# Optimization experiments

Hardware: AMD Instinct MI355X
Metric: run time of the kernel (lower is better)

## Reference

```python
import jax, jax.numpy as jnp
import numpy as np

DIM = 1024
DIM_QK = 1024
DIM_V = 1024
H = 16
SCALE = 1.0 / (DIM_QK ** 0.5)  # NOTE: module scales by sqrt(dim_qk), not sqrt(head_dim)


def setup_inputs() -> dict:
    key = jax.random.key(0)
    ks = jax.random.split(key, 12)
    B, S = 2, 2048
    q = jax.random.normal(ks[0], (B, S, DIM), jnp.float32)
    k = jax.random.normal(ks[1], (B, S, DIM), jnp.float32)
    v = jax.random.normal(ks[2], (B, S, DIM), jnp.float32)
    mask = jax.random.randint(ks[3], (B, 1, S, S), 0, 2) > 0  # True = masked
    s = 1.0 / np.sqrt(DIM)
    Wq = jax.random.uniform(ks[4], (DIM_QK, DIM), jnp.float32, -s, s)
    bq = jax.random.uniform(ks[5], (DIM_QK,), jnp.float32, -s, s)
    Wk = jax.random.uniform(ks[6], (DIM_QK, DIM), jnp.float32, -s, s)
    bk = jax.random.uniform(ks[7], (DIM_QK,), jnp.float32, -s, s)
    Wv = jax.random.uniform(ks[8], (DIM_V, DIM), jnp.float32, -s, s)
    bv = jax.random.uniform(ks[9], (DIM_V,), jnp.float32, -s, s)
    Wo = jax.random.uniform(ks[10], (DIM_V, DIM), jnp.float32, -s, s)
    bo = jax.random.uniform(ks[11], (DIM_V,), jnp.float32, -s, s)
    return {"q": q, "k": k, "v": v, "mask": mask,
            "Wq": Wq, "bq": bq, "Wk": Wk, "bk": bk,
            "Wv": Wv, "bv": bv, "Wo": Wo, "bo": bo}


def reference(q, k, v, mask, Wq, bq, Wk, bk, Wv, bv, Wo, bo):
    B, Sq, _ = q.shape
    Skv = k.shape[1]
    # projections (torch Linear: x @ W.T + b)
    qh = (q @ Wq.T + bq).reshape(B, Sq, H, DIM_QK // H).transpose(0, 2, 1, 3)   # [B,H,Sq,dk]
    kh = (k @ Wk.T + bk).reshape(B, Skv, H, DIM_QK // H).transpose(0, 2, 1, 3)  # [B,H,Skv,dk]
    vh = (v @ Wv.T + bv).reshape(B, Skv, H, DIM_V // H).transpose(0, 2, 1, 3)   # [B,H,Skv,dv]
    attn = jnp.einsum('bhqd,bhkd->bhqk', qh, kh) * SCALE
    attn = jnp.where(mask, jnp.float32(-1e20), attn)
    attn = jax.nn.softmax(attn, axis=-1)
    # dropout is identity in eval / p=0
    out = jnp.einsum('bhqk,bhkd->bhqd', attn, vh)            # [B,H,Sq,dv]
    out = out.transpose(0, 2, 1, 3).reshape(B, Sq, DIM_V)
    return out @ Wo.T + bo
```

## Files before the change

### kernel.cpp

```cpp
#include <hip/hip_runtime.h>
#include <hip/hip_bf16.h>

typedef __attribute__((ext_vector_type(8))) __bf16 bf16x8;
typedef __attribute__((ext_vector_type(4))) short short4v;
typedef __attribute__((ext_vector_type(4))) float f32x4;
typedef __attribute__((ext_vector_type(4))) unsigned int uint4v;
typedef __attribute__((ext_vector_type(2))) unsigned int uint2v;

#define S_LEN 2048
#define DIM_  1024
#define HDIM  64
#define SCALE2 0.045084441f

#define EXP2F(x) __builtin_amdgcn_exp2f(x)

#define ATTN_SWZ(row, col8) (((row) * 64) + (((col8) ^ ((row) & 7)) << 3))

__device__ __forceinline__ void async_copy16(const void* gp, void* lp) {
  __builtin_amdgcn_global_load_lds(
      (const __attribute__((address_space(1))) unsigned int*)gp,
      (__attribute__((address_space(3))) unsigned int*)lp, 16, 0, 0);
}

__device__ __forceinline__ unsigned f2bf_u(float f) {
  unsigned u = __builtin_bit_cast(unsigned, f);
  return (u + 0x7FFFu + ((u >> 16) & 1u)) >> 16;
}
__device__ __forceinline__ unsigned pack2(float a, float b) {
  return f2bf_u(a) | (f2bf_u(b) << 16);
}
__device__ __forceinline__ unsigned cvtpk(float a, float b) {
  float2 f; f.x = a; f.y = b;
  __hip_bfloat162 h = __float22bfloat162_rn(f);
  unsigned u;
  __builtin_memcpy(&u, &h, 4);
  return u;
}

__global__ __launch_bounds__(256) void cvt_kernel(
    const float* __restrict__ s0, const float* __restrict__ s1, const float* __restrict__ s2,
    const float* __restrict__ s3, const float* __restrict__ s4, const float* __restrict__ s5,
    const float* __restrict__ s6,
    __hip_bfloat16* __restrict__ d0, __hip_bfloat16* __restrict__ d1, __hip_bfloat16* __restrict__ d2,
    __hip_bfloat16* __restrict__ d3, __hip_bfloat16* __restrict__ d4, __hip_bfloat16* __restrict__ d5,
    __hip_bfloat16* __restrict__ d6,
    const int* __restrict__ mask, unsigned long long* __restrict__ bits)
{
  if (blockIdx.y == 7) {
    int wave = threadIdx.x >> 6, lane = threadIdx.x & 63;
    int gw = blockIdx.x * 4 + wave;
#pragma unroll
    for (int it = 0; it < 16; ++it) {
      int w = gw * 16 + it;
      int m = mask[(size_t)w * 64 + lane];
      unsigned long long bal = __ballot(m != 0);
      if (lane == 0) bits[w] = bal;
    }
    return;
  }
  const float* srcs[7] = {s0, s1, s2, s3, s4, s5, s6};
  __hip_bfloat16* dsts[7] = {d0, d1, d2, d3, d4, d5, d6};
  const int sizes[7] = {4194304, 4194304, 4194304, 1048576, 1048576, 1048576, 1048576};
  int rg = blockIdx.y;
  int base = (blockIdx.x * 256 + threadIdx.x) * 8;
  if (base >= sizes[rg]) return;
  const float* s = srcs[rg] + base;
  f32x4 a = *(const f32x4*)s;
  f32x4 b = *(const f32x4*)(s + 4);
  uint4v o;
  o.x = pack2(a[0], a[1]); o.y = pack2(a[2], a[3]);
  o.z = pack2(b[0], b[1]); o.w = pack2(b[2], b[3]);
  *(uint4v*)(dsts[rg] + base) = o;
}

__device__ __forceinline__ void swz(int r, int& m0, int& n0) {
  int c  = ((r & 7) << 2) | (r >> 6);
  int xl = (r >> 3) & 7;
  m0 = ((c >> 3) * 8 + xl) * 128;
  n0 = (c & 7) * 128;
}

__global__ __launch_bounds__(256) void qkv_gemm_kernel(
    const __hip_bfloat16* __restrict__ xq, const __hip_bfloat16* __restrict__ xk,
    const __hip_bfloat16* __restrict__ xv,
    const __hip_bfloat16* __restrict__ Wq, const float* __restrict__ bq,
    const __hip_bfloat16* __restrict__ Wk, const float* __restrict__ bk,
    const __hip_bfloat16* __restrict__ Wv, const float* __restrict__ bv,
    __hip_bfloat16* __restrict__ Q, __hip_bfloat16* __restrict__ Kk,
    __hip_bfloat16* __restrict__ VT)
{
  const __hip_bfloat16 *X, *W; const float* bias;
  if (blockIdx.z == 0)      { X = xq; W = Wq; bias = bq; }
  else if (blockIdx.z == 1) { X = xk; W = Wk; bias = bk; }
  else                      { X = xv; W = Wv; bias = bv; }

  constexpr int K = 1024, N = 1024;
  __shared__ alignas(16) __hip_bfloat16 As[2][128 * 32];
  __shared__ alignas(16) __hip_bfloat16 Bs[2][128 * 32];
  const int tid  = threadIdx.x;
  const int lane = tid & 63;
  const int wave = tid >> 6;
  const int t    = lane & 15;
  const int quad = lane >> 4;
  const int wm   = wave >> 1;
  const int wn   = wave & 1;
  int m0, n0;
  swz(blockIdx.x, m0, n0);

  f32x4 acc[4][4] = {};

  const int c0 = tid, c1 = 256 + tid;
  const int r0 = c0 >> 2, o0 = (c0 & 3) * 8;
  const int r1 = c1 >> 2, o1 = (c1 & 3) * 8;
  const __hip_bfloat16* xp0 = &X[(size_t)(m0 + r0) * K + o0];
  const __hip_bfloat16* xp1 = &X[(size_t)(m0 + r1) * K + o1];
  const __hip_bfloat16* wp0 = &W[(size_t)(n0 + r0) * K + o0];
  const __hip_bfloat16* wp1 = &W[(size_t)(n0 + r1) * K + o1];

  async_copy16(xp0, &As[0][c0 * 8]);
  async_copy16(xp1, &As[0][c1 * 8]);
  async_copy16(wp0, &Bs[0][c0 * 8]);
  async_copy16(wp1, &Bs[0][c1 * 8]);

  int buf = 0;
  for (int k0 = 0; k0 < K; k0 += 32) {
    __syncthreads();
    if (k0 + 32 < K) {
      int nb = buf ^ 1;
      int kn = k0 + 32;
      async_copy16(xp0 + kn, &As[nb][c0 * 8]);
      async_copy16(xp1 + kn, &As[nb][c1 * 8]);
      async_copy16(wp0 + kn, &Bs[nb][c0 * 8]);
      async_copy16(wp1 + kn, &Bs[nb][c1 * 8]);
    }
    bf16x8 a[4], b[4];
#pragma unroll
    for (int i = 0; i < 4; ++i)
      a[i] = *(const bf16x8*)&As[buf][(wm * 64 + i * 16 + t) * 32 + quad * 8];
#pragma unroll
    for (int j = 0; j < 4; ++j)
      b[j] = *(const bf16x8*)&Bs[buf][(wn * 64 + j * 16 + t) * 32 + quad * 8];
#pragma unroll
    for (int i = 0; i < 4; ++i)
#pragma unroll
      for (int j = 0; j < 4; ++j)
        acc[i][j] = __builtin_amdgcn_mfma_f32_16x16x32_bf16(a[i], b[j], acc[i][j], 0, 0, 0);
    buf ^= 1;
  }

  float bj[4];
#pragma unroll
  for (int j = 0; j < 4; ++j)
    bj[j] = bias[n0 + wn * 64 + j * 16 + t];

  if (blockIdx.z == 2) {
#pragma unroll
    for (int i = 0; i < 4; ++i)
#pragma unroll
      for (int j = 0; j < 4; ++j) {
        int m = m0 + wm * 64 + i * 16 + quad * 4;
        int n = n0 + wn * 64 + j * 16 + t;
        int bb = m >> 11, kv = m & 2047;
        int hh = n >> 6,  dv = n & 63;
        uint2v o;
        o.x = pack2(acc[i][j][0] + bj[j], acc[i][j][1] + bj[j]);
        o.y = pack2(acc[i][j][2] + bj[j], acc[i][j][3] + bj[j]);
        *(uint2v*)&VT[(size_t)(((bb * 16 + hh) * 64) + dv) * 2048 + kv] = o;
      }
  } else {
    const bool isq = (blockIdx.z == 0);
    __hip_bfloat16* Out = isq ? Q : Kk;
    const float sc = isq ? SCALE2 : 1.0f;
#pragma unroll
    for (int i = 0; i < 4; ++i)
#pragma unroll
      for (int j = 0; j < 4; ++j)
#pragma unroll
        for (int r = 0; r < 4; ++r) {
          int m = m0 + wm * 64 + i * 16 + quad * 4 + r;
          int n = n0 + wn * 64 + j * 16 + t;
          Out[(size_t)m * N + n] = __float2bfloat16((acc[i][j][r] + bj[j]) * sc);
        }
  }
}

__global__ __launch_bounds__(256) void proj_gemm_kernel(
    const __hip_bfloat16* __restrict__ X, const __hip_bfloat16* __restrict__ W,
    const float* __restrict__ bias, float* __restrict__ Out)
{
  constexpr int K = 1024, N = 1024;
  __shared__ alignas(16) __hip_bfloat16 As[2][128 * 32];
  __shared__ alignas(16) __hip_bfloat16 Bs[2][128 * 32];
  const int tid  = threadIdx.x;
  const int lane = tid & 63;
  const int wave = tid >> 6;
  const int t    = lane & 15;
  const int quad = lane >> 4;
  const int wm   = wave >> 1;
  const int wn   = wave & 1;
  int m0, n0;
  swz(blockIdx.x, m0, n0);

  f32x4 acc[4][4] = {};

  const int c0 = tid, c1 = 256 + tid;
  const int r0 = c0 >> 2, o0 = (c0 & 3) * 8;
  const int r1 = c1 >> 2, o1 = (c1 & 3) * 8;
  const __hip_bfloat16* xp0 = &X[(size_t)(m0 + r0) * K + o0];
  const __hip_bfloat16* xp1 = &X[(size_t)(m0 + r1) * K + o1];
  const __hip_bfloat16* wp0 = &W[(size_t)(n0 + r0) * K + o0];
  const __hip_bfloat16* wp1 = &W[(size_t)(n0 + r1) * K + o1];

  async_copy16(xp0, &As[0][c0 * 8]);
  async_copy16(xp1, &As[0][c1 * 8]);
  async_copy16(wp0, &Bs[0][c0 * 8]);
  async_copy16(wp1, &Bs[0][c1 * 8]);

  int buf = 0;
  for (int k0 = 0; k0 < K; k0 += 32) {
    __syncthreads();
    if (k0 + 32 < K) {
      int nb = buf ^ 1;
      int kn = k0 + 32;
      async_copy16(xp0 + kn, &As[nb][c0 * 8]);
      async_copy16(xp1 + kn, &As[nb][c1 * 8]);
      async_copy16(wp0 + kn, &Bs[nb][c0 * 8]);
      async_copy16(wp1 + kn, &Bs[nb][c1 * 8]);
    }
    bf16x8 a[4], b[4];
#pragma unroll
    for (int i = 0; i < 4; ++i)
      a[i] = *(const bf16x8*)&As[buf][(wm * 64 + i * 16 + t) * 32 + quad * 8];
#pragma unroll
    for (int j = 0; j < 4; ++j)
      b[j] = *(const bf16x8*)&Bs[buf][(wn * 64 + j * 16 + t) * 32 + quad * 8];
#pragma unroll
    for (int i = 0; i < 4; ++i)
#pragma unroll
      for (int j = 0; j < 4; ++j)
        acc[i][j] = __builtin_amdgcn_mfma_f32_16x16x32_bf16(a[i], b[j], acc[i][j], 0, 0, 0);
    buf ^= 1;
  }

  float bj[4];
#pragma unroll
  for (int j = 0; j < 4; ++j)
    bj[j] = bias[n0 + wn * 64 + j * 16 + t];
#pragma unroll
  for (int i = 0; i < 4; ++i)
#pragma unroll
    for (int j = 0; j < 4; ++j)
#pragma unroll
      for (int r = 0; r < 4; ++r) {
        int m = m0 + wm * 64 + i * 16 + quad * 4 + r;
        int n = n0 + wn * 64 + j * 16 + t;
        Out[(size_t)m * N + n] = acc[i][j][r] + bj[j];
      }
}

__global__ __launch_bounds__(256) void attn_kernel(
    const __hip_bfloat16* __restrict__ Qb,
    const __hip_bfloat16* __restrict__ Kb,
    const __hip_bfloat16* __restrict__ VT,
    const unsigned long long* __restrict__ mbits,
    __hip_bfloat16* __restrict__ Ob)
{
  const int bid = blockIdx.x;
  const int qt = (bid >> 3) & 31;
  const int g  = ((bid & 7) << 2) | (bid >> 8);
  const int h  = g & 15;
  const int b  = g >> 4;
  const int qb = qt * 64;

  __shared__ alignas(16) __hip_bfloat16 Qs[64 * 64];
  __shared__ alignas(16) __hip_bfloat16 Ks[2][64 * 64];
  __shared__ alignas(16) __hip_bfloat16 Vt[2][64 * 64];

  const int tid  = threadIdx.x;
  const int lane = tid & 63;
  const int wave = tid >> 6;
  const int t    = lane & 15;
  const int quad = lane >> 4;

  const int r0 = tid >> 3;
  const int r1 = 32 + r0;
  const int k0c = ((tid & 7) ^ (r0 & 7)) << 3;
  const int k1c = ((tid & 7) ^ (r1 & 7)) << 3;
  const __hip_bfloat16* kp0 = &Kb[((size_t)(b * S_LEN + r0)) * DIM_ + h * HDIM + k0c];
  const __hip_bfloat16* kp1 = &Kb[((size_t)(b * S_LEN + r1)) * DIM_ + h * HDIM + k1c];
  const size_t vtbase = (size_t)((b * 16 + h) * 64) * 2048;
  const __hip_bfloat16* vp0 = &VT[vtbase + (size_t)r0 * 2048 + k0c];
  const __hip_bfloat16* vp1 = &VT[vtbase + (size_t)r1 * 2048 + k1c];

  async_copy16(kp0, &Ks[0][tid * 8]);
  async_copy16(kp1, &Ks[0][(256 + tid) * 8]);
  async_copy16(vp0, &Vt[0][tid * 8]);
  async_copy16(vp1, &Vt[0][(256 + tid) * 8]);

#pragma unroll
  for (int r = 0; r < 2; ++r) {
    int c = r * 256 + tid;
    int row = c >> 3, c8 = c & 7;
    uint4 raw = *(const uint4*)&Qb[((size_t)(b * S_LEN + qb + row)) * DIM_ + h * HDIM + c8 * 8];
    *(uint4*)&Qs[ATTN_SWZ(row, c8)] = raw;
  }
  __syncthreads();

  bf16x8 qf[2];
#pragma unroll
  for (int ks = 0; ks < 2; ++ks)
    qf[ks] = *(const bf16x8*)&Qs[ATTN_SWZ(wave * 16 + t, ks * 4 + quad)];

  int koff[8];
#pragma unroll
  for (int i = 0; i < 4; ++i) {
    koff[i]     = ATTN_SWZ(i * 16 + t, quad);
    koff[4 + i] = ATTN_SWZ(i * 16 + t, 4 + quad);
  }
  int voff[16];
#pragma unroll
  for (int j = 0; j < 4; ++j)
#pragma unroll
    for (int n = 0; n < 4; ++n)
      voff[j * 4 + n] = (n * 16 + t) * 64 +
          (((j * 2 + (quad >> 1)) ^ (t & 7)) << 3) + (quad & 1) * 4;

  f32x4 lp4 = {0.f, 0.f, 0.f, 0.f};
  f32x4 o[4] = {};

  const int qg = qb + wave * 16 + t;
  const size_t mbase = ((size_t)b * S_LEN + qg) * 32;
  const int qshift = quad * 4;

#define ATTN_TILE(kvt, BUF)                                                   \
  {                                                                           \
    unsigned long long mw = mbits[mbase + (kvt)];                             \
    if ((kvt) > 0) __syncthreads();                \
    if ((kvt) + 1 < 32) {                                                     \
      size_t koffg = (size_t)((kvt) + 1) * 64 * DIM_;                         \
      int    voffg = ((kvt) + 1) * 64;                                        \
      async_copy16(kp0 + koffg, &Ks[(BUF) ^ 1][tid * 8]);                     \
      async_copy16(kp1 + koffg, &Ks[(BUF) ^ 1][(256 + tid) * 8]);             \
      async_copy16(vp0 + voffg, &Vt[(BUF) ^ 1][tid * 8]);                     \
      async_copy16(vp1 + voffg, &Vt[(BUF) ^ 1][(256 + tid) * 8]);             \
    }                                                                         \
    __builtin_amdgcn_s_setprio(1);                                            \
    unsigned long long mwq = mw >> qshift;                                    \
    unsigned mlo = (unsigned)mwq, mhi = (unsigned)(mwq >> 32);                \
    unsigned mqv[4] = {mlo & 0xFu, (mlo >> 16) & 0xFu,                        \
                       mhi & 0xFu, (mhi >> 16) & 0xFu};                       \
    float e[4][4];                                                            \
    _Pragma("unroll")                                                         \
    for (int i = 0; i < 4; ++i) {                                             \
      f32x4 z = {};                                                           \
      bf16x8 a0 = *(const bf16x8*)&Ks[BUF][koff[i]];                          \
      z = __builtin_amdgcn_mfma_f32_16x16x32_bf16(a0, qf[0], z, 0, 0, 0);     \
      bf16x8 a1 = *(const bf16x8*)&Ks[BUF][koff[4 + i]];                      \
      z = __builtin_amdgcn_mfma_f32_16x16x32_bf16(a1, qf[1], z, 0, 0, 0);     \
      _Pragma("unroll")                                                       \
      for (int r = 0; r < 4; ++r) {                                           \
        float v = ((mqv[i] >> r) & 1u) ? -1e20f : z[r];                       \
        float ex = EXP2F(v);                                                  \
        e[i][r] = ex;                                                         \
        lp4[r] += ex;                                                         \
      }                                                                       \
    }                                                                         \
    short4v pf[4];                                                            \
    _Pragma("unroll")                                                         \
    for (int j = 0; j < 4; ++j) {                                             \
      uint2v pk;                                                              \
      pk.x = cvtpk(e[j][0], e[j][1]);                                         \
      pk.y = cvtpk(e[j][2], e[j][3]);                                         \
      pf[j] = __builtin_bit_cast(short4v, pk);                                \
    }                                                                         \
    _Pragma("unroll")                                                         \
    for (int j = 0; j < 4; ++j)                                               \
      _Pragma("unroll")                                                       \
      for (int n = 0; n < 4; ++n) {                                           \
        short4v va = *(const short4v*)&Vt[BUF][voff[j * 4 + n]];              \
        o[n] = __builtin_amdgcn_mfma_f32_16x16x16bf16_1k(va, pf[j], o[n],     \
                                                         0, 0, 0);            \
      }                                                                       \
    __builtin_amdgcn_s_setprio(0);                                            \
  }

  ATTN_TILE(0, 0)
  for (int kvt = 1; kvt < 31; kvt += 2) {
    ATTN_TILE(kvt, 1)
    ATTN_TILE(kvt + 1, 0)
  }
  ATTN_TILE(31, 1)
#undef ATTN_TILE

  float lp = (lp4[0] + lp4[1]) + (lp4[2] + lp4[3]);
  lp += __shfl_xor(lp, 16, 64);
  lp += __shfl_xor(lp, 32, 64);
  float rl = 1.0f / lp;

  __hip_bfloat16* Ts = Qs;
  __syncthreads();
#pragma unroll
  for (int n = 0; n < 4; ++n) {
    uint2v pk;
    pk.x = cvtpk(o[n][0] * rl, o[n][1] * rl);
    pk.y = cvtpk(o[n][2] * rl, o[n][3] * rl);
    *(uint2v*)&Ts[(wave * 16 + t) * 64 +
                  (((n * 2 + (quad >> 1)) ^ (t & 7)) << 3) + (quad & 1) * 4] = pk;
  }
  __syncthreads();
  {
    int row = tid >> 2;
    int b0  = (tid & 3) * 2;
    uint4 x0 = *(const uint4*)&Ts[row * 64 + ((b0 ^ (row & 7)) << 3)];
    uint4 x1 = *(const uint4*)&Ts[row * 64 + (((b0 + 1) ^ (row & 7)) << 3)];
    int d0 = (tid & 3) * 16;
    __hip_bfloat16* dst = &Ob[((size_t)(b * S_LEN + qb + row)) * DIM_ + h * HDIM + d0];
    *(uint4*)dst = x0;
    *(uint4*)(dst + 8) = x1;
  }
}

extern "C" void kernel_launch(void* const* d_in, const int* in_sizes, int n_in,
                              void* d_out, int out_size, void* d_ws, size_t ws_size,
                              hipStream_t stream) {
  const float* q  = (const float*)d_in[0];
  const float* k  = (const float*)d_in[1];
  const float* v  = (const float*)d_in[2];
  const int*   mk = (const int*)d_in[3];
  const float* Wq = (const float*)d_in[4];
  const float* bq = (const float*)d_in[5];
  const float* Wk = (const float*)d_in[6];
  const float* bk = (const float*)d_in[7];
  const float* Wv = (const float*)d_in[8];
  const float* bv = (const float*)d_in[9];
  const float* Wo = (const float*)d_in[10];
  const float* bo = (const float*)d_in[11];
  float* out = (float*)d_out;

  char* ws = (char*)d_ws;
  const size_t MB = 1024 * 1024;
  __hip_bfloat16* Qb  = (__hip_bfloat16*)(ws);
  __hip_bfloat16* Kb  = (__hip_bfloat16*)(ws + 8  * MB);
  __hip_bfloat16* VTb = (__hip_bfloat16*)(ws + 16 * MB);
  __hip_bfloat16* Ob  = (__hip_bfloat16*)(ws + 24 * MB);
  __hip_bfloat16* xqb = (__hip_bfloat16*)(ws + 32 * MB);
  __hip_bfloat16* xkb = (__hip_bfloat16*)(ws + 40 * MB);
  __hip_bfloat16* xvb = (__hip_bfloat16*)(ws + 48 * MB);
  __hip_bfloat16* Wqb = (__hip_bfloat16*)(ws + 56 * MB);
  __hip_bfloat16* Wkb = (__hip_bfloat16*)(ws + 58 * MB);
  __hip_bfloat16* Wvb = (__hip_bfloat16*)(ws + 60 * MB);
  __hip_bfloat16* Wob = (__hip_bfloat16*)(ws + 62 * MB);
  unsigned long long* mbits = (unsigned long long*)(ws + 64 * MB);

  cvt_kernel<<<dim3(2048, 8), 256, 0, stream>>>(q, k, v, Wq, Wk, Wv, Wo,
                                                xqb, xkb, xvb, Wqb, Wkb, Wvb, Wob,
                                                mk, mbits);
  qkv_gemm_kernel<<<dim3(256, 1, 3), 256, 0, stream>>>(xqb, xkb, xvb,
                                                       Wqb, bq, Wkb, bk, Wvb, bv,
                                                       Qb, Kb, VTb);
  attn_kernel<<<dim3(1024), 256, 0, stream>>>(Qb, Kb, VTb, mbits, Ob);
  proj_gemm_kernel<<<dim3(256), 256, 0, stream>>>(Ob, Wob, bo, out);
}
```

Measured before the change: 260.6 us.

## Process 128 query rows per attention block to reuse K/V tiles

Each attention workgroup now covers 128 query rows instead of 64, with every wave handling two 16-row query sub-tiles that share the same K fragments and V loads from LDS. This halves the global K/V traffic and the LDS fragment reads per query row, and it halves the grid to 512 blocks. In exchange, register pressure rises from doubled accumulators and cached K fragments, and the smaller grid may underfill the 256 CUs.

```diff
diff --git a/kernel.cpp b/kernel.cpp
--- a/kernel.cpp
+++ b/kernel.cpp
@@ -266,13 +266,13 @@
     __hip_bfloat16* __restrict__ Ob)
 {
   const int bid = blockIdx.x;
-  const int qt = (bid >> 3) & 31;
-  const int g  = ((bid & 7) << 2) | (bid >> 8);
+  const int qt = (bid >> 3) & 15;
+  const int g  = ((bid & 7) << 2) | (bid >> 7);
   const int h  = g & 15;
   const int b  = g >> 4;
-  const int qb = qt * 64;
-
-  __shared__ alignas(16) __hip_bfloat16 Qs[64 * 64];
+  const int qb = qt * 128;
+
+  __shared__ alignas(16) __hip_bfloat16 Qs[128 * 64];
   __shared__ alignas(16) __hip_bfloat16 Ks[2][64 * 64];
   __shared__ alignas(16) __hip_bfloat16 Vt[2][64 * 64];
 
@@ -298,7 +298,7 @@
   async_copy16(vp1, &Vt[0][(256 + tid) * 8]);
 
 #pragma unroll
-  for (int r = 0; r < 2; ++r) {
+  for (int r = 0; r < 4; ++r) {
     int c = r * 256 + tid;
     int row = c >> 3, c8 = c & 7;
     uint4 raw = *(const uint4*)&Qb[((size_t)(b * S_LEN + qb + row)) * DIM_ + h * HDIM + c8 * 8];
@@ -306,10 +306,12 @@
   }
   __syncthreads();
 
-  bf16x8 qf[2];
-#pragma unroll
-  for (int ks = 0; ks < 2; ++ks)
-    qf[ks] = *(const bf16x8*)&Qs[ATTN_SWZ(wave * 16 + t, ks * 4 + quad)];
+  bf16x8 qf[2][2];
+#pragma unroll
+  for (int hh = 0; hh < 2; ++hh)
+#pragma unroll
+    for (int ks = 0; ks < 2; ++ks)
+      qf[hh][ks] = *(const bf16x8*)&Qs[ATTN_SWZ(wave * 32 + hh * 16 + t, ks * 4 + quad)];
 
   int koff[8];
 #pragma unroll
@@ -325,16 +327,19 @@
       voff[j * 4 + n] = (n * 16 + t) * 64 +
           (((j * 2 + (quad >> 1)) ^ (t & 7)) << 3) + (quad & 1) * 4;
 
-  f32x4 lp4 = {0.f, 0.f, 0.f, 0.f};
-  f32x4 o[4] = {};
-
-  const int qg = qb + wave * 16 + t;
-  const size_t mbase = ((size_t)b * S_LEN + qg) * 32;
+  f32x4 lpa = {0.f, 0.f, 0.f, 0.f};
+  f32x4 lpb = {0.f, 0.f, 0.f, 0.f};
+  f32x4 oa[4] = {};
+  f32x4 ob[4] = {};
+
+  const size_t mbase0 = ((size_t)b * S_LEN + qb + wave * 32 + t) * 32;
+  const size_t mbase1 = mbase0 + 16 * 32;
   const int qshift = quad * 4;
 
 #define ATTN_TILE(kvt, BUF)                                                   \
   {                                                                           \
-    unsigned long long mw = mbits[mbase + (kvt)];                             \
+    unsigned long long mw0 = mbits[mbase0 + (kvt)];                           \
+    unsigned long long mw1 = mbits[mbase1 + (kvt)];                           \
     if ((kvt) > 0) __syncthreads();                \
     if ((kvt) + 1 < 32) {                                                     \
       size_t koffg = (size_t)((kvt) + 1) * 64 * DIM_;                         \
@@ -345,41 +350,62 @@
       async_copy16(vp1 + voffg, &Vt[(BUF) ^ 1][(256 + tid) * 8]);             \
     }                                                                         \
     __builtin_amdgcn_s_setprio(1);                                            \
-    unsigned long long mwq = mw >> qshift;                                    \
-    unsigned mlo = (unsigned)mwq, mhi = (unsigned)(mwq >> 32);                \
-    unsigned mqv[4] = {mlo & 0xFu, (mlo >> 16) & 0xFu,                        \
-                       mhi & 0xFu, (mhi >> 16) & 0xFu};                       \
-    float e[4][4];                                                            \
+    unsigned long long mwq0 = mw0 >> qshift;                                  \
+    unsigned long long mwq1 = mw1 >> qshift;                                  \
+    unsigned m0lo = (unsigned)mwq0, m0hi = (unsigned)(mwq0 >> 32);            \
+    unsigned m1lo = (unsigned)mwq1, m1hi = (unsigned)(mwq1 >> 32);            \
+    unsigned mqv0[4] = {m0lo & 0xFu, (m0lo >> 16) & 0xFu,                     \
+                        m0hi & 0xFu, (m0hi >> 16) & 0xFu};                    \
+    unsigned mqv1[4] = {m1lo & 0xFu, (m1lo >> 16) & 0xFu,                     \
+                        m1hi & 0xFu, (m1hi >> 16) & 0xFu};                    \
+    bf16x8 kf[8];                                                             \
+    _Pragma("unroll")                                                         \
+    for (int i = 0; i < 4; ++i) {                                             \
+      kf[i]     = *(const bf16x8*)&Ks[BUF][koff[i]];                          \
+      kf[4 + i] = *(const bf16x8*)&Ks[BUF][koff[4 + i]];                      \
+    }                                                                         \
+    short4v pf0[4], pf1[4];                                                   \
     _Pragma("unroll")                                                         \
     for (int i = 0; i < 4; ++i) {                                             \
       f32x4 z = {};                                                           \
-      bf16x8 a0 = *(const bf16x8*)&Ks[BUF][koff[i]];                          \
-      z = __builtin_amdgcn_mfma_f32_16x16x32_bf16(a0, qf[0], z, 0, 0, 0);     \
-      bf16x8 a1 = *(const bf16x8*)&Ks[BUF][koff[4 + i]];                      \
-      z = __builtin_amdgcn_mfma_f32_16x16x32_bf16(a1, qf[1], z, 0, 0, 0);     \
-      _Pragma("unroll")                                                       \
-      for (int r = 0; r < 4; ++r) {                                           \
-        float v = ((mqv[i] >> r) & 1u) ? -1e20f : z[r];                       \
-        float ex = EXP2F(v);                                                  \
-        e[i][r] = ex;                                                         \
-        lp4[r] += ex;                                                         \
-      }                                                                       \
+      z = __builtin_amdgcn_mfma_f32_16x16x32_bf16(kf[i], qf[0][0], z, 0, 0, 0);\
+      z = __builtin_amdgcn_mfma_f32_16x16x32_bf16(kf[4 + i], qf[0][1], z, 0, 0, 0);\
+      float e0, e1, e2, e3;                                                   \
+      e0 = EXP2F((mqv0[i] & 1u) ? -1e20f : z[0]);                             \
+      e1 = EXP2F((mqv0[i] & 2u) ? -1e20f : z[1]);                             \
+      e2 = EXP2F((mqv0[i] & 4u) ? -1e20f : z[2]);                             \
+      e3 = EXP2F((mqv0[i] & 8u) ? -1e20f : z[3]);                             \
+      lpa[0] += e0; lpa[1] += e1; lpa[2] += e2; lpa[3] += e3;                 \
+      uint2v pk;                                                              \
+      pk.x = cvtpk(e0, e1);                                                   \
+      pk.y = cvtpk(e2, e3);                                                   \
+      pf0[i] = __builtin_bit_cast(short4v, pk);                               \
     }                                                                         \
-    short4v pf[4];                                                            \
     _Pragma("unroll")                                                         \
-    for (int j = 0; j < 4; ++j) {                                             \
+    for (int i = 0; i < 4; ++i) {                                             \
+      f32x4 z = {};                                                           \
+      z = __builtin_amdgcn_mfma_f32_16x16x32_bf16(kf[i], qf[1][0], z, 0, 0, 0);\
+      z = __builtin_amdgcn_mfma_f32_16x16x32_bf16(kf[4 + i], qf[1][1], z, 0, 0, 0);\
+      float e0, e1, e2, e3;                                                   \
+      e0 = EXP2F((mqv1[i] & 1u) ? -1e20f : z[0]);                             \
+      e1 = EXP2F((mqv1[i] & 2u) ? -1e20f : z[1]);                             \
+      e2 = EXP2F((mqv1[i] & 4u) ? -1e20f : z[2]);                             \
+      e3 = EXP2F((mqv1[i] & 8u) ? -1e20f : z[3]);                             \
+      lpb[0] += e0; lpb[1] += e1; lpb[2] += e2; lpb[3] += e3;                 \
       uint2v pk;                                                              \
-      pk.x = cvtpk(e[j][0], e[j][1]);                                         \
-      pk.y = cvtpk(e[j][2], e[j][3]);                                         \
-      pf[j] = __builtin_bit_cast(short4v, pk);                                \
+      pk.x = cvtpk(e0, e1);                                                   \
+      pk.y = cvtpk(e2, e3);                                                   \
+      pf1[i] = __builtin_bit_cast(short4v, pk);                               \
     }                                                                         \
     _Pragma("unroll")                                                         \
     for (int j = 0; j < 4; ++j)                                               \
       _Pragma("unroll")                                                       \
       for (int n = 0; n < 4; ++n) {                                           \
         short4v va = *(const short4v*)&Vt[BUF][voff[j * 4 + n]];              \
-        o[n] = __builtin_amdgcn_mfma_f32_16x16x16bf16_1k(va, pf[j], o[n],     \
-                                                         0, 0, 0);            \
+        oa[n] = __builtin_amdgcn_mfma_f32_16x16x16bf16_1k(va, pf0[j], oa[n],  \
+                                                          0, 0, 0);           \
+        ob[n] = __builtin_amdgcn_mfma_f32_16x16x16bf16_1k(va, pf1[j], ob[n],  \
+                                                          0, 0, 0);           \
       }                                                                       \
     __builtin_amdgcn_s_setprio(0);                                            \
   }
@@ -392,31 +418,40 @@
   ATTN_TILE(31, 1)
 #undef ATTN_TILE
 
-  float lp = (lp4[0] + lp4[1]) + (lp4[2] + lp4[3]);
-  lp += __shfl_xor(lp, 16, 64);
-  lp += __shfl_xor(lp, 32, 64);
-  float rl = 1.0f / lp;
+  float la = (lpa[0] + lpa[1]) + (lpa[2] + lpa[3]);
+  la += __shfl_xor(la, 16, 64);
+  la += __shfl_xor(la, 32, 64);
+  float rla = 1.0f / la;
+  float lb = (lpb[0] + lpb[1]) + (lpb[2] + lpb[3]);
+  lb += __shfl_xor(lb, 16, 64);
+  lb += __shfl_xor(lb, 32, 64);
+  float rlb = 1.0f / lb;
 
   __hip_bfloat16* Ts = Qs;
   __syncthreads();
 #pragma unroll
   for (int n = 0; n < 4; ++n) {
+    int cswz = (((n * 2 + (quad >> 1)) ^ (t & 7)) << 3) + (quad & 1) * 4;
     uint2v pk;
-    pk.x = cvtpk(o[n][0] * rl, o[n][1] * rl);
-    pk.y = cvtpk(o[n][2] * rl, o[n][3] * rl);
-    *(uint2v*)&Ts[(wave * 16 + t) * 64 +
-                  (((n * 2 + (quad >> 1)) ^ (t & 7)) << 3) + (quad & 1) * 4] = pk;
+    pk.x = cvtpk(oa[n][0] * rla, oa[n][1] * rla);
+    pk.y = cvtpk(oa[n][2] * rla, oa[n][3] * rla);
+    *(uint2v*)&Ts[(wave * 32 + t) * 64 + cswz] = pk;
+    uint2v pk2;
+    pk2.x = cvtpk(ob[n][0] * rlb, ob[n][1] * rlb);
+    pk2.y = cvtpk(ob[n][2] * rlb, ob[n][3] * rlb);
+    *(uint2v*)&Ts[(wave * 32 + 16 + t) * 64 + cswz] = pk2;
   }
   __syncthreads();
   {
-    int row = tid >> 2;
-    int b0  = (tid & 3) * 2;
-    uint4 x0 = *(const uint4*)&Ts[row * 64 + ((b0 ^ (row & 7)) << 3)];
-    uint4 x1 = *(const uint4*)&Ts[row * 64 + (((b0 + 1) ^ (row & 7)) << 3)];
-    int d0 = (tid & 3) * 16;
-    __hip_bfloat16* dst = &Ob[((size_t)(b * S_LEN + qb + row)) * DIM_ + h * HDIM + d0];
-    *(uint4*)dst = x0;
-    *(uint4*)(dst + 8) = x1;
+    int row = tid >> 1;
+    int half = tid & 1;
+    __hip_bfloat16* dst = &Ob[((size_t)(b * S_LEN + qb + row)) * DIM_ + h * HDIM + half * 32];
+#pragma unroll
+    for (int bb = 0; bb < 4; ++bb) {
+      int blk = half * 4 + bb;
+      uint4 x = *(const uint4*)&Ts[row * 64 + ((blk ^ (row & 7)) << 3)];
+      *(uint4*)(dst + bb * 8) = x;
+    }
   }
 }
 
@@ -458,6 +493,6 @@
   qkv_gemm_kernel<<<dim3(256, 1, 3), 256, 0, stream>>>(xqb, xkb, xvb,
                                                        Wqb, bq, Wkb, bk, Wvb, bv,
                                                        Qb, Kb, VTb);
-  attn_kernel<<<dim3(1024), 256, 0, stream>>>(Qb, Kb, VTb, mbits, Ob);
+  attn_kernel<<<dim3(512), 256, 0, stream>>>(Qb, Kb, VTb, mbits, Ob);
   proj_gemm_kernel<<<dim3(256), 256, 0, stream>>>(Ob, Wob, bo, out);
 }
```

After: 264.0 us. No clear change (+1.3%).
